# Performance work log

Hardware: AMD Instinct MI355X
Metric: run time of the kernel (lower is better)

## Reference

```python
import jax, jax.numpy as jnp
import numpy as np
import math

B, S, D, DFF, E, K = 8, 2048, 1024, 4096, 8, 2
CAP_FACTOR = 1.6   # n_experts=8 > 6 branch in __init__
NOISE_STD = 0.02   # n_experts=8 > 6 branch in __init__


def setup_inputs() -> dict:
    key = jax.random.key(0)
    ks = jax.random.split(key, 6)
    x = jax.random.normal(ks[0], (B, S, D), jnp.float32)
    noise = jax.random.normal(ks[1], (B * S, E), jnp.float32)  # router exploration noise
    router_w = jax.random.normal(ks[2], (E, D), jnp.float32) * 0.02
    router_b = jnp.zeros((E,), jnp.float32)
    w1 = jax.random.normal(ks[3], (E, D, DFF), jnp.float32) * 0.02
    b1 = jnp.zeros((E, DFF), jnp.float32)
    w2 = jax.random.normal(ks[4], (E, DFF, D), jnp.float32) * 0.02
    b2 = jnp.zeros((E, D), jnp.float32)
    return {"x": x, "noise": noise, "router_w": router_w, "router_b": router_b,
            "w1": w1, "b1": b1, "w2": w2, "b2": b2}


def reference(x, noise, router_w, router_b, w1, b1, w2, b2):
    b, s, d = x.shape
    T = b * s
    x_flat = x.reshape(T, d)
    # Router: logits + gaussian exploration noise (randn_like * noise_std)
    logits = x_flat @ router_w.T + router_b + noise * NOISE_STD
    probs = jax.nn.softmax(logits, axis=-1)
    _, topk_idx = jax.lax.top_k(probs, K)  # [T, K]
    capacity = math.ceil(T * CAP_FACTOR / E)  # static
    # Pad row T: gathers of dropped slots read zeros; scatters to it are discarded.
    x_pad = jnp.concatenate([x_flat, jnp.zeros((1, d), x_flat.dtype)], axis=0)
    out = jnp.zeros((T + 1, d), x_flat.dtype)
    # NOTE: original writes (not weighted-adds) expert outputs; later experts
    # overwrite earlier ones for tokens routed to both. Loop order matters.
    for i in range(E):
        mask = (topk_idx == i).any(axis=-1)  # [T]
        # first `capacity` tokens in order (matches token_indices[:capacity]);
        # padded slots get index T.
        idx = jnp.nonzero(mask, size=capacity, fill_value=T)[0]
        inp = x_pad[idx]                                   # [cap, d]
        h = jax.nn.gelu(inp @ w1[i] + b1[i], approximate=False)
        eo = h @ w2[i] + b2[i]                             # [cap, d]
        out = out.at[idx].set(eo)
    return out[:T].reshape(b, s, d)
```

## Files before the change

### kernel.cpp

```cpp
#include <hip/hip_runtime.h>
#include <math.h>

#define T_TOK   16384
#define DMODEL  1024
#define DFF     4096
#define NEXP    8
#define CAPACITY 3277
#define CAP_PAD  3328

typedef unsigned short u16;
typedef __attribute__((ext_vector_type(8))) __bf16 bf16x8;
typedef __attribute__((ext_vector_type(4))) float  f32x4;

#define W1T_OFF   0ull
#define W2T_OFF   67108864ull
#define XG_OFF    134217728ull
#define H_OFF     171966464ull
#define TOPK_OFF  322961408ull
#define CCNT_OFF  323092480ull
#define CBASE_OFF 323096576ull
#define LISTS_OFF 323100672ull
#define CNT_OFF   323207168ull
#define OFFS_OFF  323207200ull
#define PCNT_OFF  323207296ull
#define ACC_OFF   323207424ull

__device__ __forceinline__ u16 f2bf(float x) {
  union { float f; unsigned u; } v; v.f = x;
  unsigned r = v.u + 0x7fffu + ((v.u >> 16) & 1u);
  return (u16)(r >> 16);
}

__device__ __forceinline__ void async_cp16(const void* g, void* l) {
  __builtin_amdgcn_global_load_lds((const __attribute__((address_space(1))) void*)g,
                                   (__attribute__((address_space(3))) void*)l,
                                   16, 0, 0);
}

__device__ __forceinline__ void barrier_fence() {
  asm volatile("" ::: "memory");
  __builtin_amdgcn_s_barrier();
  asm volatile("" ::: "memory");
}

__global__ __launch_bounds__(256) void transpose_cvt64(const float* __restrict__ src,
                                                       u16* __restrict__ dst, int R, int C) {
  int tilesC = C >> 6;
  int per_e = (R >> 6) * tilesC;
  int bid = blockIdx.x;
  int e = bid / per_e, rem = bid % per_e;
  int rt = rem / tilesC, ct = rem % tilesC;
  const float* s = src + (size_t)e * R * C;
  u16* d = dst + (size_t)e * R * C;
  __shared__ u16 tile[64][70];
  int tid = threadIdx.x;
  int rr = tid >> 4;
  int c4 = (tid & 15) << 2;
#pragma unroll
  for (int i = 0; i < 4; ++i) {
    int r = rr + i * 16;
    float4 v = *(const float4*)(s + (size_t)(rt*64 + r) * C + ct*64 + c4);
    unsigned lo = (unsigned)f2bf(v.x) | ((unsigned)f2bf(v.y) << 16);
    unsigned hi = (unsigned)f2bf(v.z) | ((unsigned)f2bf(v.w) << 16);
    *(unsigned*)&tile[r][c4]     = lo;
    *(unsigned*)&tile[r][c4 + 2] = hi;
  }
  __syncthreads();
#pragma unroll
  for (int k = 0; k < 2; ++k) {
    int idx = k*256 + tid;
    int c  = idx >> 3;
    int rc = (idx & 7) << 3;
    union { u16 u[8]; uint4 v; } pk;
#pragma unroll
    for (int j = 0; j < 8; ++j) pk.u[j] = tile[rc + j][c];
    *(uint4*)(d + (size_t)(ct*64 + c) * R + rt*64 + rc) = pk.v;
  }
}

__global__ __launch_bounds__(256) void router_topk(const float* __restrict__ x,
    const float* __restrict__ rw, const float* __restrict__ rb,
    const float* __restrict__ noise, int* __restrict__ topk) {
  int w = threadIdx.x >> 6, lane = threadIdx.x & 63;
  int t = blockIdx.x * 4 + w;
  const float* xr = x + (size_t)t * DMODEL;
  double acc[NEXP];
#pragma unroll
  for (int e = 0; e < NEXP; ++e) acc[e] = 0.0;
  for (int c = lane; c < DMODEL; c += 64) {
    float xv = xr[c];
#pragma unroll
    for (int e = 0; e < NEXP; ++e) acc[e] += (double)xv * (double)rw[e*DMODEL + c];
  }
#pragma unroll
  for (int e = 0; e < NEXP; ++e) {
#pragma unroll
    for (int off = 32; off > 0; off >>= 1) acc[e] += __shfl_down(acc[e], off, 64);
  }
  if (lane == 0) {
    double best = -1e300, sec = -1e300; int bi = 0, si = 0;
#pragma unroll
    for (int e = 0; e < NEXP; ++e) {
      double v = acc[e] + (double)rb[e] + (double)noise[(size_t)t*NEXP + e] * 0.02;
      if (v > best)     { sec = best; si = bi; best = v; bi = e; }
      else if (v > sec) { sec = v; si = e; }
    }
    topk[2*t] = bi; topk[2*t+1] = si;
  }
}

__global__ __launch_bounds__(128) void chunk_count(const int* __restrict__ topk,
                                                   int* __restrict__ ccnt) {
  int tid = threadIdx.x, lane = tid & 63, w = tid >> 6;
  int t = blockIdx.x*128 + tid;
  int i0 = topk[2*t], i1 = topk[2*t+1];
  __shared__ int cnt[2][NEXP];
#pragma unroll
  for (int e = 0; e < NEXP; ++e) {
    unsigned long long bal = __ballot((i0 == e) || (i1 == e));
    if (lane == 0) cnt[w][e] = __popcll(bal);
  }
  __syncthreads();
  if (tid < NEXP) ccnt[blockIdx.x*NEXP + tid] = cnt[0][tid] + cnt[1][tid];
}

__global__ void chunk_prefix(const int* __restrict__ ccnt, int* __restrict__ cbase) {
  int e = threadIdx.x;
  if (e < NEXP) {
    int run = 0;
    for (int c = 0; c < 128; ++c) { cbase[c*NEXP + e] = run; run += ccnt[c*NEXP + e]; }
  }
}

__global__ __launch_bounds__(128) void assign_compact(const int* __restrict__ topk,
    const int* __restrict__ cbase, int* __restrict__ counts, int* __restrict__ lists,
    int* __restrict__ accept) {
  int chunk = blockIdx.x, tid = threadIdx.x;
  int lane = tid & 63, w = tid >> 6;
  int t = chunk*128 + tid;
  int i0 = topk[2*t], i1 = topk[2*t+1];
  __shared__ int w0cnt[NEXP];
  unsigned long long below = (1ull << lane) - 1ull;
#pragma unroll
  for (int e = 0; e < NEXP; ++e) {
    unsigned long long bal = __ballot((i0 == e) || (i1 == e));
    if (w == 0 && lane == 0) w0cnt[e] = __popcll(bal);
  }
  __syncthreads();
  int fin = -1;
#pragma unroll
  for (int e = 0; e < NEXP; ++e) {
    bool m = (i0 == e) || (i1 == e);
    unsigned long long bal = __ballot(m);
    int rank = cbase[chunk*NEXP + e] + (w ? w0cnt[e] : 0) + __popcll(bal & below);
    if (m && rank < CAPACITY) fin = e;
  }
  accept[t] = (fin >= 0) ? 1 : 0;
#pragma unroll
  for (int e = 0; e < NEXP; ++e) {
    bool m = (fin == e);
    unsigned long long bal = __ballot(m);
    int c = __popcll(bal);
    if (c) {
      int leader = __ffsll((unsigned long long)bal) - 1;
      int base = 0;
      if (lane == leader) base = atomicAdd(&counts[e], c);
      base = __shfl(base, leader, 64);
      if (m) lists[e*CAP_PAD + base + __popcll(bal & below)] = t;
    }
  }
}

__global__ void calc_offsets(const int* __restrict__ counts, int* __restrict__ offs,
                             int* __restrict__ pcnt) {
  if (threadIdx.x == 0) {
    int run = 0;
    for (int e = 0; e < NEXP; ++e) {
      offs[e] = run;
      int pc = ((counts[e] + 255) >> 8) << 8;
      pcnt[e] = pc;
      run += pc;
    }
    offs[NEXP] = run;
  }
}

__global__ __launch_bounds__(256) void zero_dropped(const int* __restrict__ accept,
                                                    float* __restrict__ out) {
  int lane = threadIdx.x & 63, w = threadIdx.x >> 6;
  for (int tok = blockIdx.x*4 + w; tok < T_TOK; tok += gridDim.x*4) {
    if (!accept[tok]) {
      float4 z = make_float4(0.f, 0.f, 0.f, 0.f);
      float4* p = (float4*)(out + (size_t)tok * DMODEL);
#pragma unroll
      for (int i = 0; i < 4; ++i) p[lane + i*64] = z;
    }
  }
}

__global__ __launch_bounds__(128) void gather_x(const float* __restrict__ x,
    const int* __restrict__ lists, const int* __restrict__ counts,
    const int* __restrict__ offs, const int* __restrict__ pcnt, u16* __restrict__ xg) {
  int tid = threadIdx.x;
  for (int idx = blockIdx.x; idx < NEXP*CAP_PAD; idx += gridDim.x) {
    int e = idx / CAP_PAD, r = idx % CAP_PAD;
    if (r >= pcnt[e]) continue;
    unsigned long long* dst = (unsigned long long*)(xg + (size_t)(offs[e] + r) * DMODEL);
    if (r < counts[e]) {
      const float4* src = (const float4*)(x + (size_t)lists[e*CAP_PAD + r] * DMODEL);
#pragma unroll
      for (int i = 0; i < 2; ++i) {
        float4 v = src[tid + i*128];
        unsigned long long pk = (unsigned long long)f2bf(v.x)
                              | ((unsigned long long)f2bf(v.y) << 16)
                              | ((unsigned long long)f2bf(v.z) << 32)
                              | ((unsigned long long)f2bf(v.w) << 48);
        dst[tid + i*128] = pk;
      }
    } else {
#pragma unroll
      for (int i = 0; i < 2; ++i) dst[tid + i*128] = 0ull;
    }
  }
}


template<int S>
__device__ __forceinline__ void stage_half(const u16* __restrict__ g, int row0, int k0,
                                           u16* tile, int half, int tid) {
  int wid  = tid >> 6;
  int rloc = tid >> 3;
  int cb   = (tid & 7) << 4;
  int scb  = cb ^ ((rloc & 7) << 4);
#pragma unroll
  for (int j = 0; j < 2; ++j) {
    int r = half*128 + j*64 + rloc;
    const u16* src = g + (size_t)(row0 + r) * S + k0 + (scb >> 1);
    u16* dst = tile + half*8192 + j*4096 + wid*512;
    async_cp16(src, dst);
  }
}

__device__ __forceinline__ bf16x8 ldsfrag(const u16* tile, int r, int cb) {
  int a = r*128 + (cb ^ ((r & 7) << 4));
  return *(const bf16x8*)((const char*)tile + a);
}

template<int KELEM, int NTOT, int EPI>
__global__ __launch_bounds__(512, 2) void ffn_gemm8(
    const u16* __restrict__ Abase, const u16* __restrict__ Btall,
    const float* __restrict__ bias,
    const int* __restrict__ offs, const int* __restrict__ pcnt,
    const int* __restrict__ counts, const int* __restrict__ lists,
    u16* __restrict__ Hout, float* __restrict__ Fout) {
  constexpr int NKT = KELEM / 64;
  int e = blockIdx.z, mt = blockIdx.y, nt = blockIdx.x;
  int pc = pcnt[e];
  int m0 = mt * 256;
  if (m0 >= pc) return;
  int n0 = nt * 256;
  int tid = threadIdx.x, lane = tid & 63, wid = tid >> 6;
  int wm = wid >> 2, wn = wid & 3;
  const u16* A = Abase + (size_t)offs[e] * KELEM;
  const u16* B = Btall + (size_t)e * NTOT * KELEM;
  __shared__ __align__(16) u16 lds[2][2][16384];

  stage_half<KELEM>(A, m0, 0,  (u16*)lds[0][0], 0, tid);
  stage_half<KELEM>(A, m0, 0,  (u16*)lds[0][0], 1, tid);
  stage_half<KELEM>(B, n0, 0,  (u16*)lds[0][1], 0, tid);
  stage_half<KELEM>(B, n0, 0,  (u16*)lds[0][1], 1, tid);
  stage_half<KELEM>(B, n0, 64, (u16*)lds[1][1], 0, tid);
  stage_half<KELEM>(B, n0, 64, (u16*)lds[1][1], 1, tid);
  asm volatile("s_waitcnt vmcnt(4)" ::: "memory");
  barrier_fence();

  int frow = lane & 15;
  int fk   = (lane >> 4) << 4;
  f32x4 acc[8][4] = {};

#pragma unroll 2
  for (int t = 0; t < NKT; ++t) {
    int cur = t & 1;
    u16* As_ = (u16*)lds[cur][0];
    u16* Bs_ = (u16*)lds[cur][1];
    u16* An_ = (u16*)lds[cur ^ 1][0];
    bf16x8 a[4][2], bb[2][2][2];

#pragma unroll
    for (int f = 0; f < 4; ++f)
#pragma unroll
      for (int kk = 0; kk < 2; ++kk)
        a[f][kk] = ldsfrag(As_, wm*128 + f*16 + frow, kk*64 + fk);
#pragma unroll
    for (int f = 0; f < 2; ++f)
#pragma unroll
      for (int kk = 0; kk < 2; ++kk)
        bb[0][f][kk] = ldsfrag(Bs_, wn*64 + f*16 + frow, kk*64 + fk);
    if (t + 1 < NKT) stage_half<KELEM>(A, m0, (t+1)*64, An_, 0, tid);
    barrier_fence();
    __builtin_amdgcn_s_setprio(1);
#pragma unroll
    for (int f = 0; f < 4; ++f)
#pragma unroll
      for (int g = 0; g < 2; ++g)
#pragma unroll
        for (int kk = 0; kk < 2; ++kk)
          acc[f][g] = __builtin_amdgcn_mfma_f32_16x16x32_bf16(a[f][kk], bb[0][g][kk], acc[f][g], 0, 0, 0);
    __builtin_amdgcn_s_setprio(0);
    barrier_fence();

#pragma unroll
    for (int f = 0; f < 2; ++f)
#pragma unroll
      for (int kk = 0; kk < 2; ++kk)
        bb[1][f][kk] = ldsfrag(Bs_, wn*64 + (2+f)*16 + frow, kk*64 + fk);
    if (t + 1 < NKT) stage_half<KELEM>(A, m0, (t+1)*64, An_, 1, tid);
    barrier_fence();
    __builtin_amdgcn_s_setprio(1);
#pragma unroll
    for (int f = 0; f < 4; ++f)
#pragma unroll
      for (int g = 0; g < 2; ++g)
#pragma unroll
        for (int kk = 0; kk < 2; ++kk)
          acc[f][2+g] = __builtin_amdgcn_mfma_f32_16x16x32_bf16(a[f][kk], bb[1][g][kk], acc[f][2+g], 0, 0, 0);
    __builtin_amdgcn_s_setprio(0);
    barrier_fence();

#pragma unroll
    for (int f = 0; f < 4; ++f)
#pragma unroll
      for (int kk = 0; kk < 2; ++kk)
        a[f][kk] = ldsfrag(As_, wm*128 + 64 + f*16 + frow, kk*64 + fk);
    if (t + 2 < NKT) stage_half<KELEM>(B, n0, (t+2)*64, Bs_, 0, tid);
    barrier_fence();
    __builtin_amdgcn_s_setprio(1);
#pragma unroll
    for (int f = 0; f < 4; ++f)
#pragma unroll
      for (int g = 0; g < 2; ++g)
#pragma unroll
        for (int kk = 0; kk < 2; ++kk)
          acc[4+f][g] = __builtin_amdgcn_mfma_f32_16x16x32_bf16(a[f][kk], bb[0][g][kk], acc[4+f][g], 0, 0, 0);
    __builtin_amdgcn_s_setprio(0);
    barrier_fence();

    if (t + 2 < NKT) stage_half<KELEM>(B, n0, (t+2)*64, Bs_, 1, tid);
    barrier_fence();
    __builtin_amdgcn_s_setprio(1);
#pragma unroll
    for (int f = 0; f < 4; ++f)
#pragma unroll
      for (int g = 0; g < 2; ++g)
#pragma unroll
        for (int kk = 0; kk < 2; ++kk)
          acc[4+f][2+g] = __builtin_amdgcn_mfma_f32_16x16x32_bf16(a[f][kk], bb[1][g][kk], acc[4+f][2+g], 0, 0, 0);
    __builtin_amdgcn_s_setprio(0);
    if (t + 2 < NKT)      asm volatile("s_waitcnt vmcnt(4)" ::: "memory");
    else if (t + 1 < NKT) asm volatile("s_waitcnt vmcnt(0)" ::: "memory");
    barrier_fence();
  }

  if constexpr (EPI == 0) {
    const float* be = bias + e * NTOT;
    u16* H = Hout + (size_t)offs[e] * NTOT;
    char* mybuf = (char*)lds + wid * 16384;
    float bv[4];
#pragma unroll
    for (int g = 0; g < 4; ++g) bv[g] = be[n0 + wn*64 + g*16 + frow];
    int r4 = (lane >> 4) * 4;
#pragma unroll
    for (int f = 0; f < 8; ++f)
#pragma unroll
      for (int g = 0; g < 4; ++g)
#pragma unroll
        for (int r = 0; r < 4; ++r) {
          float v = acc[f][g][r] + bv[g];
          float gl = 0.5f * v * (1.0f + erff(v * 0.70710678118654752f));
          int rr = f*16 + r4 + r;
          int cb = (g*16 + frow) * 2;
          *(u16*)(mybuf + rr*128 + (cb ^ ((rr & 7) << 4))) = f2bf(gl);
        }
    asm volatile("s_waitcnt lgkmcnt(0)" ::: "memory");
#pragma unroll
    for (int rb = 0; rb < 8; ++rb)
#pragma unroll
      for (int kk = 0; kk < 2; ++kk) {
        int rr = rb*16 + frow;
        int c8 = kk*4 + (lane >> 4);
        bf16x8 vv = *(const bf16x8*)(mybuf + rr*128 + ((c8*16) ^ ((rr & 7) << 4)));
        *(bf16x8*)(H + (size_t)(m0 + wm*128 + rr) * NTOT + n0 + wn*64 + c8*8) = vv;
      }
  } else {
    int cnt = counts[e];
    const float* be = bias + e * NTOT;
    const int* le = lists + e * CAP_PAD;
    float* mybuf = (float*)((u16*)lds + wid * 2304);
    float bv[4];
#pragma unroll
    for (int g = 0; g < 4; ++g) bv[g] = be[n0 + wn*64 + g*16 + frow];
    int r4 = (lane >> 4) * 4;
#pragma unroll
    for (int f = 0; f < 8; ++f) {
#pragma unroll
      for (int g = 0; g < 4; ++g)
#pragma unroll
        for (int r = 0; r < 4; ++r)
          mybuf[(r4 + r) * 68 + g*16 + frow] = acc[f][g][r] + bv[g];
      asm volatile("s_waitcnt lgkmcnt(0)" ::: "memory");
      int row = lane >> 2, cg = lane & 3;
      int grow = m0 + wm*128 + f*16 + row;
      if (grow < cnt) {
        int tk = le[grow];
        float* po = Fout + (size_t)tk * DMODEL + n0 + wn*64 + cg*16;
        const float* pb = mybuf + row*68 + cg*16;
#pragma unroll
        for (int j = 0; j < 4; ++j)
          *(f32x4*)(po + j*4) = *(const f32x4*)(pb + j*4);
      }
      asm volatile("s_waitcnt lgkmcnt(0)" ::: "memory");
    }
  }
}

extern "C" void kernel_launch(void* const* d_in, const int* in_sizes, int n_in,
                              void* d_out, int out_size, void* d_ws, size_t ws_size,
                              hipStream_t stream) {
  const float* x     = (const float*)d_in[0];
  const float* noise = (const float*)d_in[1];
  const float* rw    = (const float*)d_in[2];
  const float* rb    = (const float*)d_in[3];
  const float* w1    = (const float*)d_in[4];
  const float* b1    = (const float*)d_in[5];
  const float* w2    = (const float*)d_in[6];
  const float* b2    = (const float*)d_in[7];
  float* out = (float*)d_out;
  char* ws = (char*)d_ws;

  u16* w1t   = (u16*)(ws + W1T_OFF);
  u16* w2t   = (u16*)(ws + W2T_OFF);
  u16* xg    = (u16*)(ws + XG_OFF);
  u16* hbuf  = (u16*)(ws + H_OFF);
  int* topk  = (int*)(ws + TOPK_OFF);
  int* ccnt  = (int*)(ws + CCNT_OFF);
  int* cbase = (int*)(ws + CBASE_OFF);
  int* lists = (int*)(ws + LISTS_OFF);
  int* cnts  = (int*)(ws + CNT_OFF);
  int* offs  = (int*)(ws + OFFS_OFF);
  int* pcnt  = (int*)(ws + PCNT_OFF);
  int* accfl = (int*)(ws + ACC_OFF);

  hipMemsetAsync(cnts, 0, NEXP * sizeof(int), stream);

  transpose_cvt64<<<NEXP*(DMODEL/64)*(DFF/64), 256, 0, stream>>>(w1, w1t, DMODEL, DFF);
  transpose_cvt64<<<NEXP*(DFF/64)*(DMODEL/64), 256, 0, stream>>>(w2, w2t, DFF, DMODEL);
  router_topk<<<T_TOK/4, 256, 0, stream>>>(x, rw, rb, noise, topk);
  chunk_count<<<128, 128, 0, stream>>>(topk, ccnt);
  chunk_prefix<<<1, 64, 0, stream>>>(ccnt, cbase);
  assign_compact<<<128, 128, 0, stream>>>(topk, cbase, cnts, lists, accfl);
  calc_offsets<<<1, 64, 0, stream>>>(cnts, offs, pcnt);
  zero_dropped<<<512, 256, 0, stream>>>(accfl, out);
  gather_x<<<4096, 128, 0, stream>>>(x, lists, cnts, offs, pcnt, xg);
  ffn_gemm8<DMODEL, DFF, 0><<<dim3(DFF/256, CAP_PAD/256, NEXP), 512, 0, stream>>>(
      xg, w1t, b1, offs, pcnt, cnts, lists, hbuf, nullptr);
  ffn_gemm8<DFF, DMODEL, 1><<<dim3(DMODEL/256, CAP_PAD/256, NEXP), 512, 0, stream>>>(
      hbuf, w2t, b2, offs, pcnt, cnts, lists, nullptr, out);
}
```

Baseline: 726.4 us.

## Remap GEMM block ids for XCD-local weight reuse and merge weight transposes

Measured after the change: 735.9 us. About the same (+1.3%).

```diff
diff --git a/kernel.cpp b/kernel.cpp
--- a/kernel.cpp
+++ b/kernel.cpp
@@ -43,38 +43,46 @@
   asm volatile("" ::: "memory");
 }
 
-__global__ __launch_bounds__(256) void transpose_cvt64(const float* __restrict__ src,
-                                                       u16* __restrict__ dst, int R, int C) {
-  int tilesC = C >> 6;
-  int per_e = (R >> 6) * tilesC;
-  int bid = blockIdx.x;
-  int e = bid / per_e, rem = bid % per_e;
-  int rt = rem / tilesC, ct = rem % tilesC;
-  const float* s = src + (size_t)e * R * C;
-  u16* d = dst + (size_t)e * R * C;
+__global__ __launch_bounds__(256) void transpose_cvt_all(
+    const float* __restrict__ w1, const float* __restrict__ w2,
+    u16* __restrict__ w1t, u16* __restrict__ w2t) {
   __shared__ u16 tile[64][70];
   int tid = threadIdx.x;
   int rr = tid >> 4;
   int c4 = (tid & 15) << 2;
-#pragma unroll
-  for (int i = 0; i < 4; ++i) {
-    int r = rr + i * 16;
-    float4 v = *(const float4*)(s + (size_t)(rt*64 + r) * C + ct*64 + c4);
-    unsigned lo = (unsigned)f2bf(v.x) | ((unsigned)f2bf(v.y) << 16);
-    unsigned hi = (unsigned)f2bf(v.z) | ((unsigned)f2bf(v.w) << 16);
-    *(unsigned*)&tile[r][c4]     = lo;
-    *(unsigned*)&tile[r][c4 + 2] = hi;
-  }
-  __syncthreads();
-#pragma unroll
-  for (int k = 0; k < 2; ++k) {
-    int idx = k*256 + tid;
-    int c  = idx >> 3;
-    int rc = (idx & 7) << 3;
-    union { u16 u[8]; uint4 v; } pk;
-#pragma unroll
-    for (int j = 0; j < 8; ++j) pk.u[j] = tile[rc + j][c];
-    *(uint4*)(d + (size_t)(ct*64 + c) * R + rt*64 + rc) = pk.v;
+  const int JOBS1 = NEXP * (DMODEL/64) * (DFF/64);
+  const int JOBS  = 2 * JOBS1;
+  for (int job = blockIdx.x; job < JOBS; job += gridDim.x) {
+    const float* src; u16* dst; int R, C; int j = job;
+    if (j < JOBS1) { src = w1; dst = w1t; R = DMODEL; C = DFF; }
+    else           { src = w2; dst = w2t; R = DFF; C = DMODEL; j -= JOBS1; }
+    int tilesC = C >> 6;
+    int per_e = (R >> 6) * tilesC;
+    int e = j / per_e, rem = j % per_e;
+    int rt = rem / tilesC, ct = rem % tilesC;
+    const float* s = src + (size_t)e * R * C;
+    u16* d = dst + (size_t)e * R * C;
+#pragma unroll
+    for (int i = 0; i < 4; ++i) {
+      int r = rr + i * 16;
+      float4 v = *(const float4*)(s + (size_t)(rt*64 + r) * C + ct*64 + c4);
+      unsigned lo = (unsigned)f2bf(v.x) | ((unsigned)f2bf(v.y) << 16);
+      unsigned hi = (unsigned)f2bf(v.z) | ((unsigned)f2bf(v.w) << 16);
+      *(unsigned*)&tile[r][c4]     = lo;
+      *(unsigned*)&tile[r][c4 + 2] = hi;
+    }
+    __syncthreads();
+#pragma unroll
+    for (int k = 0; k < 2; ++k) {
+      int idx = k*256 + tid;
+      int c  = idx >> 3;
+      int rc = (idx & 7) << 3;
+      union { u16 u[8]; uint4 v; } pk;
+#pragma unroll
+      for (int jj = 0; jj < 8; ++jj) pk.u[jj] = tile[rc + jj][c];
+      *(uint4*)(d + (size_t)(ct*64 + c) * R + rt*64 + rc) = pk.v;
+    }
+    __syncthreads();
   }
 }
 
@@ -254,7 +262,22 @@
     const int* __restrict__ counts, const int* __restrict__ lists,
     u16* __restrict__ Hout, float* __restrict__ Fout) {
   constexpr int NKT = KELEM / 64;
-  int e = blockIdx.z, mt = blockIdx.y, nt = blockIdx.x;
+  int bid = blockIdx.x;
+  int xcd = bid & 7;
+  int s   = bid >> 3;
+  int e, mt, nt;
+  if constexpr (NTOT == DFF) {
+    int pair = s >> 1, half = s & 1;
+    e  = pair & 7;
+    mt = pair >> 3;
+    nt = xcd*2 + half;
+  } else {
+    int grp = s >> 2, sub = s & 3;
+    int g = xcd + grp*8;
+    e  = g / 13;
+    mt = g % 13;
+    nt = sub;
+  }
   int pc = pcnt[e];
   int m0 = mt * 256;
   if (m0 >= pc) return;
@@ -452,8 +475,7 @@
 
   hipMemsetAsync(cnts, 0, NEXP * sizeof(int), stream);
 
-  transpose_cvt64<<<NEXP*(DMODEL/64)*(DFF/64), 256, 0, stream>>>(w1, w1t, DMODEL, DFF);
-  transpose_cvt64<<<NEXP*(DFF/64)*(DMODEL/64), 256, 0, stream>>>(w2, w2t, DFF, DMODEL);
+  transpose_cvt_all<<<2048, 256, 0, stream>>>(w1, w2, w1t, w2t);
   router_topk<<<T_TOK/4, 256, 0, stream>>>(x, rw, rb, noise, topk);
   chunk_count<<<128, 128, 0, stream>>>(topk, ccnt);
   chunk_prefix<<<1, 64, 0, stream>>>(ccnt, cbase);
@@ -461,8 +483,8 @@
   calc_offsets<<<1, 64, 0, stream>>>(cnts, offs, pcnt);
   zero_dropped<<<512, 256, 0, stream>>>(accfl, out);
   gather_x<<<4096, 128, 0, stream>>>(x, lists, cnts, offs, pcnt, xg);
-  ffn_gemm8<DMODEL, DFF, 0><<<dim3(DFF/256, CAP_PAD/256, NEXP), 512, 0, stream>>>(
+  ffn_gemm8<DMODEL, DFF, 0><<<NEXP*13*(DFF/256), 512, 0, stream>>>(
       xg, w1t, b1, offs, pcnt, cnts, lists, hbuf, nullptr);
-  ffn_gemm8<DFF, DMODEL, 1><<<dim3(DMODEL/256, CAP_PAD/256, NEXP), 512, 0, stream>>>(
+  ffn_gemm8<DFF, DMODEL, 1><<<NEXP*13*(DMODEL/256), 512, 0, stream>>>(
       hbuf, w2t, b2, offs, pcnt, cnts, lists, nullptr, out);
 }
```
